# Kernel optimization log

Measured on AMD Instinct MI355X. Metric: run time of the kernel, lower is better.

Reference implementation:

```python
import jax, jax.numpy as jnp
import numpy as np

BETA = 1.0
B, S, D = 4, 4096, 1024


def setup_inputs() -> dict:
    key = jax.random.key(0)
    k_x, k_q, k_k, k_v = jax.random.split(key, 4)
    scale = 1.0 / np.sqrt(D)  # nn.Linear-like init scale
    x = jax.random.normal(k_x, (B, S, D), dtype=jnp.float32)
    Wq = jax.random.uniform(k_q, (D, D), dtype=jnp.float32, minval=-scale, maxval=scale)
    Wk = jax.random.uniform(k_k, (D, D), dtype=jnp.float32, minval=-scale, maxval=scale)
    Wv = jax.random.uniform(k_v, (D, D), dtype=jnp.float32, minval=-scale, maxval=scale)
    return {"x": x, "Wq": Wq, "Wk": Wk, "Wv": Wv}


def reference(x, Wq, Wk, Wv):
    # nn.Linear(bias=False): y = x @ W.T
    q = jnp.einsum('bsd,ed->bse', x, Wq)
    k = jnp.einsum('bsd,ed->bse', x, Wk)
    v = jnp.einsum('bsd,ed->bse', x, Wv)
    scores = jnp.einsum('bqd,bkd->bqk', q, k)          # [B, S, S]
    attn = jax.nn.softmax(BETA * scores, axis=-1)
    attended = jnp.einsum('bqk,bkd->bqd', attn, v)
    y = attended + x
    return y / jnp.linalg.norm(y, axis=-1, keepdims=True)
```

## Files before the change

### kernel.cpp

```cpp
#include <hip/hip_runtime.h>

typedef unsigned short u16;
typedef _Float16 half8 __attribute__((ext_vector_type(8)));
typedef __attribute__((ext_vector_type(4))) float f32x4;

constexpr int NB = 4;
constexpr int S  = 4096;
constexpr int D  = 1024;

__device__ __forceinline__ u16 h2u(_Float16 h) {
    union { _Float16 h; u16 u; } v; v.h = h; return v.u;
}

__device__ __forceinline__ void async16(const void* g, void* l) {
    __builtin_amdgcn_global_load_lds(
        (const __attribute__((address_space(1))) unsigned int*)g,
        (__attribute__((address_space(3))) unsigned int*)l, 16, 0, 0);
}

#define BAR()  __builtin_amdgcn_s_barrier()
#define SFEN() __builtin_amdgcn_sched_barrier(0)

#define MF(AF, BF, QM, QN)                                                     \
  do {                                                                         \
    _Pragma("unroll") for (int m_ = 0; m_ < 4; ++m_)                           \
    _Pragma("unroll") for (int n_ = 0; n_ < 2; ++n_)                           \
    _Pragma("unroll") for (int k_ = 0; k_ < 2; ++k_)                           \
      acc[(QM)*4 + m_][(QN)*2 + n_] = __builtin_amdgcn_mfma_f32_16x16x32_f16(  \
          AF[m_][k_], BF[n_][k_], acc[(QM)*4 + m_][(QN)*2 + n_], 0, 0, 0);     \
  } while (0)

#define GHALF(RA, RB, OA, OB, KO, KN)                                          \
  {                                               \
    _Pragma("unroll") for (int m_ = 0; m_ < 4; ++m_) {                         \
      a0[m_][0] = rdA(RA, 0, m_, 0); a0[m_][1] = rdA(RA, 0, m_, 1); }          \
    _Pragma("unroll") for (int n_ = 0; n_ < 2; ++n_) {                         \
      b0[n_][0] = rdB(RB, 0, n_, 0); b0[n_][1] = rdB(RB, 0, n_, 1); }          \
    issue(Am, OA, rsA + 64, KO);                                               \
    BAR();                                                                     \
    __builtin_amdgcn_s_setprio(1); MF(a0, b0, 0, 0);                           \
    __builtin_amdgcn_s_setprio(0);                                             \
    asm volatile("s_waitcnt vmcnt(6)" ::: "memory");                           \
    BAR(); SFEN();                                                             \
                                                  \
    _Pragma("unroll") for (int n_ = 0; n_ < 2; ++n_) {                         \
      b1[n_][0] = rdB(RB, 1, n_, 0); b1[n_][1] = rdB(RB, 1, n_, 1); }          \
    issue(Bm, OB, rsB + 32, KO);                                               \
    BAR();                                                                     \
    __builtin_amdgcn_s_setprio(1); MF(a0, b1, 0, 1);                           \
    __builtin_amdgcn_s_setprio(0);                                             \
    BAR(); SFEN();                                                             \
                                                  \
    _Pragma("unroll") for (int m_ = 0; m_ < 4; ++m_) {                         \
      a1[m_][0] = rdA(RA, 1, m_, 0); a1[m_][1] = rdA(RA, 1, m_, 1); }          \
    issue(Am, RA, rsA, KN);                                                    \
    BAR();                                                                     \
    __builtin_amdgcn_s_setprio(1); MF(a1, b0, 1, 0);                           \
    __builtin_amdgcn_s_setprio(0);                                             \
    BAR(); SFEN();                                                             \
                                                  \
    issue(Bm, RB, rsB, KN);                                                    \
    BAR();                                                                     \
    __builtin_amdgcn_s_setprio(1); MF(a1, b1, 1, 1);                           \
    __builtin_amdgcn_s_setprio(0);                                             \
    asm volatile("s_waitcnt vmcnt(8)" ::: "memory");                           \
    BAR(); SFEN();                                                             \
  }

__device__ __forceinline__ void gemm256(
    const u16* __restrict__ Am, const u16* __restrict__ Bm, const int K,
    u16* lds, f32x4 acc[8][4])
{
    const int tid  = threadIdx.x;
    const int lane = tid & 63;
    const int w    = tid >> 6;
    const int wm   = w >> 2;
    const int wn   = w & 3;
    const int quad = lane >> 4;
    const int lrow = lane & 15;
    const int s7   = lrow & 7;
    const int rl   = lane >> 3;
    const int gc8  = ((lane & 7) ^ rl) * 8;
    const int rsA  = ((w >> 2) << 7) + ((w & 3) << 4);
    const int rsB  = ((w >> 1) << 6) + ((w & 1) << 4);

    u16* const As0 = lds;
    u16* const Bs0 = lds + 16384;
    u16* const As1 = lds + 32768;
    u16* const Bs1 = lds + 49152;

    auto issue = [&](const u16* M, u16* dst, int rs, int k0) {
        async16(M + (size_t)(rs + rl) * K + k0 + gc8,
                dst + (size_t)(rs)     * 64 + (size_t)lane * 8);
        async16(M + (size_t)(rs + 8 + rl) * K + k0 + gc8,
                dst + (size_t)(rs + 8) * 64 + (size_t)lane * 8);
    };
    auto rdA = [&](const u16* buf, int qm, int m, int kk) -> half8 {
        return *(const half8*)(buf + (wm * 128 + qm * 64 + m * 16 + lrow) * 64
                                   + (((kk << 2) + quad) ^ s7) * 8);
    };
    auto rdB = [&](const u16* buf, int qn, int n, int kk) -> half8 {
        return *(const half8*)(buf + (wn * 64 + qn * 32 + n * 16 + lrow) * 64
                                   + (((kk << 2) + quad) ^ s7) * 8);
    };

    issue(Am, As0, rsA,      0);
    issue(Bm, Bs0, rsB,      0);
    issue(Am, As0, rsA + 64, 0);
    issue(Bm, Bs0, rsB + 32, 0);
    issue(Am, As1, rsA,      64);
    issue(Bm, Bs1, rsB,      64);
    asm volatile("s_waitcnt vmcnt(8)" ::: "memory");
    BAR(); SFEN();

    half8 a0[4][2], a1[4][2], b0[2][2], b1[2][2];
    const int kmask = K - 1;
    const int NI = K >> 7;
    for (int it = 0; it < NI; ++it) {
        const int kb  = it << 7;
        const int t1k = (kb + 64)  & kmask;
        const int t2k = (kb + 128) & kmask;
        const int t3k = (kb + 192) & kmask;
        GHALF(As0, Bs0, As1, Bs1, t1k, t2k)
        GHALF(As1, Bs1, As0, Bs0, t2k, t3k)
    }
}

__global__ __launch_bounds__(256) void cvt_kernel(
    const float* __restrict__ in, u16* __restrict__ out, int n8)
{
    const int i = blockIdx.x * 256 + threadIdx.x;
    if (i >= n8) return;
    const float4 a = *(const float4*)(in + (size_t)i * 8);
    const float4 b = *(const float4*)(in + (size_t)i * 8 + 4);
    half8 h;
    h[0] = (_Float16)a.x; h[1] = (_Float16)a.y;
    h[2] = (_Float16)a.z; h[3] = (_Float16)a.w;
    h[4] = (_Float16)b.x; h[5] = (_Float16)b.y;
    h[6] = (_Float16)b.z; h[7] = (_Float16)b.w;
    *(half8*)(out + (size_t)i * 8) = h;
}

__global__ __launch_bounds__(512, 2) void qkv_kernel(
    const u16* __restrict__ x16, const u16* __restrict__ W16,
    u16* __restrict__ Q, u16* __restrict__ Kb, u16* __restrict__ V)
{
    __shared__ __align__(16) u16 lds[65536];
    const int tile_m = blockIdx.x * 256;
    const int tile_n = blockIdx.y * 256;
    const u16* W = W16 + (size_t)blockIdx.z * D * D;
    u16* out = (blockIdx.z == 0) ? Q : (blockIdx.z == 1) ? Kb : V;

    f32x4 acc[8][4];
#pragma unroll
    for (int i = 0; i < 8; ++i)
#pragma unroll
        for (int j = 0; j < 4; ++j) acc[i][j] = (f32x4)0.0f;

    gemm256(x16 + (size_t)tile_m * D, W + (size_t)tile_n * D, D, lds, acc);

    const int tid = threadIdx.x, lane = tid & 63, w = tid >> 6;
    const int quad = lane >> 4, lrow = lane & 15;
    const int wm = w >> 2, wn = w & 3;
#pragma unroll
    for (int mi = 0; mi < 8; ++mi)
#pragma unroll
        for (int r = 0; r < 4; ++r) {
            const int row = tile_m + wm * 128 + mi * 16 + quad * 4 + r;
#pragma unroll
            for (int ni = 0; ni < 4; ++ni) {
                const int col = tile_n + wn * 64 + ni * 16 + lrow;
                out[(size_t)row * D + col] = h2u((_Float16)acc[mi][ni][r]);
            }
        }
}

__global__ __launch_bounds__(256) void transpose_v(
    const u16* __restrict__ V, u16* __restrict__ Vt)
{
    __shared__ u16 t[64][72];
    const int sg = blockIdx.x * 64;
    const int b  = sg >> 12;
    const int s0 = sg & (S - 1);
    const int e0 = blockIdx.y * 64;
    const int tid = threadIdx.x;
#pragma unroll
    for (int p = 0; p < 2; ++p) {
        const int v  = tid + 256 * p;
        const int sr = v >> 3, sc = (v & 7) * 8;
        half8 vec = *(const half8*)(V + (size_t)(sg + sr) * D + e0 + sc);
        *(half8*)&t[sr][sc] = vec;
    }
    __syncthreads();
#pragma unroll
    for (int p = 0; p < 2; ++p) {
        const int v  = tid + 256 * p;
        const int e  = v >> 3, s8 = (v & 7) * 8;
        u16 o[8];
#pragma unroll
        for (int j = 0; j < 8; ++j) o[j] = t[s8 + j][e];
        *(uint4*)(Vt + (size_t)b * D * S + (size_t)(e0 + e) * S + s0 + s8) = *(const uint4*)o;
    }
}

__global__ __launch_bounds__(512, 2) void scores_kernel(
    const u16* __restrict__ Q, const u16* __restrict__ Kb, u16* __restrict__ P)
{
    __shared__ __align__(16) u16 lds[65536];
    const int b = blockIdx.z;
    const int tile_m = blockIdx.x * 256;
    const int tile_n = blockIdx.y * 256;
    const u16* Ab = Q  + (size_t)b * S * D + (size_t)tile_m * D;
    const u16* Bv = Kb + (size_t)b * S * D + (size_t)tile_n * D;

    f32x4 acc[8][4];
#pragma unroll
    for (int i = 0; i < 8; ++i)
#pragma unroll
        for (int j = 0; j < 4; ++j) acc[i][j] = (f32x4)0.0f;

    gemm256(Ab, Bv, D, lds, acc);

    u16* Pb = P + (size_t)b * S * S;
    const int tid = threadIdx.x, lane = tid & 63, w = tid >> 6;
    const int quad = lane >> 4, lrow = lane & 15;
    const int wm = w >> 2, wn = w & 3;
#pragma unroll
    for (int mi = 0; mi < 8; ++mi)
#pragma unroll
        for (int r = 0; r < 4; ++r) {
            const int row = tile_m + wm * 128 + mi * 16 + quad * 4 + r;
#pragma unroll
            for (int ni = 0; ni < 4; ++ni) {
                const int col = tile_n + wn * 64 + ni * 16 + lrow;
                Pb[(size_t)row * S + col] = h2u((_Float16)acc[mi][ni][r]);
            }
        }
}

__global__ __launch_bounds__(256) void softmax_kernel(u16* __restrict__ P)
{
    const size_t row = blockIdx.x;
    u16* p = P + row * S;
    const int tid = threadIdx.x;

    half8 h0 = *(const half8*)(p + tid * 16);
    half8 h1 = *(const half8*)(p + tid * 16 + 8);
    float v[16];
#pragma unroll
    for (int i = 0; i < 8; ++i) { v[i] = (float)h0[i]; v[8 + i] = (float)h1[i]; }

    float m = v[0];
#pragma unroll
    for (int i = 1; i < 16; ++i) m = fmaxf(m, v[i]);
#pragma unroll
    for (int off = 32; off > 0; off >>= 1) m = fmaxf(m, __shfl_xor(m, off));

    __shared__ float redm[4], reds[4];
    const int wid = tid >> 6;
    if ((tid & 63) == 0) redm[wid] = m;
    __syncthreads();
    m = fmaxf(fmaxf(redm[0], redm[1]), fmaxf(redm[2], redm[3]));

    float e[16], s = 0.f;
#pragma unroll
    for (int i = 0; i < 16; ++i) { e[i] = __expf(v[i] - m); s += e[i]; }
#pragma unroll
    for (int off = 32; off > 0; off >>= 1) s += __shfl_xor(s, off);
    if ((tid & 63) == 0) reds[wid] = s;
    __syncthreads();
    s = reds[0] + reds[1] + reds[2] + reds[3];
    const float inv = 1.0f / s;

#pragma unroll
    for (int i = 0; i < 8; ++i) {
        h0[i] = (_Float16)(e[i] * inv);
        h1[i] = (_Float16)(e[8 + i] * inv);
    }
    *(half8*)(p + tid * 16)     = h0;
    *(half8*)(p + tid * 16 + 8) = h1;
}

__global__ __launch_bounds__(512, 2) void pv_kernel(
    const u16* __restrict__ P, const u16* __restrict__ Vt,
    const float* __restrict__ x, float* __restrict__ y)
{
    __shared__ __align__(16) u16 lds[65536];
    const int b = blockIdx.z;
    const int tile_m = blockIdx.x * 256;
    const int tile_n = blockIdx.y * 256;
    const u16* Ab = P  + (size_t)b * S * S + (size_t)tile_m * S;
    const u16* Bv = Vt + (size_t)b * D * S + (size_t)tile_n * S;

    f32x4 acc[8][4];
#pragma unroll
    for (int i = 0; i < 8; ++i)
#pragma unroll
        for (int j = 0; j < 4; ++j) acc[i][j] = (f32x4)0.0f;

    gemm256(Ab, Bv, S, lds, acc);

    const int tid = threadIdx.x, lane = tid & 63, w = tid >> 6;
    const int quad = lane >> 4, lrow = lane & 15;
    const int wm = w >> 2, wn = w & 3;

#pragma unroll
    for (int mi = 0; mi < 8; ++mi)
#pragma unroll
        for (int r = 0; r < 4; ++r) {
            const int row = tile_m + wm * 128 + mi * 16 + quad * 4 + r;
            const size_t base = ((size_t)b * S + row) * D;
#pragma unroll
            for (int ni = 0; ni < 4; ++ni) {
                const int col = tile_n + wn * 64 + ni * 16 + lrow;
                y[base + col] = acc[mi][ni][r] + x[base + col];
            }
        }
}

__global__ __launch_bounds__(256) void normalize_kernel(float* __restrict__ y)
{
    const size_t row = blockIdx.x;
    const int tid = threadIdx.x;
    float4* p = (float4*)(y + row * D) + tid;

    float4 v = *p;
    float ss = v.x * v.x + v.y * v.y + v.z * v.z + v.w * v.w;
#pragma unroll
    for (int off = 32; off > 0; off >>= 1) ss += __shfl_xor(ss, off);

    __shared__ float red[4];
    const int wid = tid >> 6;
    if ((tid & 63) == 0) red[wid] = ss;
    __syncthreads();
    const float inv = rsqrtf(red[0] + red[1] + red[2] + red[3]);

    v.x *= inv; v.y *= inv; v.z *= inv; v.w *= inv;
    *p = v;
}

extern "C" void kernel_launch(void* const* d_in, const int* in_sizes, int n_in,
                              void* d_out, int out_size, void* d_ws, size_t ws_size,
                              hipStream_t stream) {
    const float* x  = (const float*)d_in[0];
    const float* Wq = (const float*)d_in[1];
    const float* Wk = (const float*)d_in[2];
    const float* Wv = (const float*)d_in[3];
    float* out = (float*)d_out;

    char* ws = (char*)d_ws;
    const size_t MB = 1ull << 20;
    u16* Q   = (u16*)(ws);
    u16* Kb  = (u16*)(ws + 32 * MB);
    u16* Vt  = (u16*)(ws + 64 * MB);
    u16* P   = (u16*)(ws + 96 * MB);
    u16* V   = P;
    u16* x16 = Vt;
    u16* W16 = (u16*)(ws + 218 * MB);

    dim3 blk(256);
    dim3 blk2(512);
    cvt_kernel <<<dim3(NB * S * D / 8 / 256), blk, 0, stream>>>(x,  x16, NB * S * D / 8);
    cvt_kernel <<<dim3(D * D / 8 / 256), blk, 0, stream>>>(Wq, W16,             D * D / 8);
    cvt_kernel <<<dim3(D * D / 8 / 256), blk, 0, stream>>>(Wk, W16 + (size_t)D * D, D * D / 8);
    cvt_kernel <<<dim3(D * D / 8 / 256), blk, 0, stream>>>(Wv, W16 + (size_t)2 * D * D, D * D / 8);

    qkv_kernel    <<<dim3(NB * S / 256, D / 256, 3), blk2, 0, stream>>>(x16, W16, Q, Kb, V);
    transpose_v   <<<dim3(NB * S / 64, D / 64), blk, 0, stream>>>(V, Vt);
    scores_kernel <<<dim3(S / 256, S / 256, NB), blk2, 0, stream>>>(Q, Kb, P);
    softmax_kernel<<<dim3(NB * S), blk, 0, stream>>>(P);
    pv_kernel     <<<dim3(S / 256, D / 256, NB), blk2, 0, stream>>>(P, Vt, x, out);
    normalize_kernel<<<dim3(NB * S), blk, 0, stream>>>(out);
}
```

Measured before the change: 537.8 us.

## Restructure GEMM main loop barriers, precompute LDS pointers, and swizzle block order for XCDs

The GEMM inner loop now issues LDS fragment reads for the next sub-step before each barrier instead of after, removes one barrier per quarter-step, and waits with a tighter vmcnt. LDS read addresses are precomputed as per-thread base pointers with constant offsets, replacing the per-read index arithmetic. All three GEMM kernels remap the linear block id so consecutive blocks on the same XCD handle neighbouring tiles, aiming for better L2 reuse. Fewer barriers raise the risk of LDS read/write races if the async-load waits are not sufficient.

Result: slower. 549.7 us (+2.2%).

```diff
diff --git a/kernel.cpp b/kernel.cpp
--- a/kernel.cpp
+++ b/kernel.cpp
@@ -30,40 +30,40 @@
           AF[m_][k_], BF[n_][k_], acc[(QM)*4 + m_][(QN)*2 + n_], 0, 0, 0);     \
   } while (0)
 
-#define GHALF(RA, RB, OA, OB, KO, KN)                                          \
-  {                                               \
-    _Pragma("unroll") for (int m_ = 0; m_ < 4; ++m_) {                         \
-      a0[m_][0] = rdA(RA, 0, m_, 0); a0[m_][1] = rdA(RA, 0, m_, 1); }          \
-    _Pragma("unroll") for (int n_ = 0; n_ < 2; ++n_) {                         \
-      b0[n_][0] = rdB(RB, 0, n_, 0); b0[n_][1] = rdB(RB, 0, n_, 1); }          \
-    issue(Am, OA, rsA + 64, KO);                                               \
-    BAR();                                                                     \
+#define RDA(dst, bp0, bp1, qm)                                                 \
+  _Pragma("unroll") for (int m_ = 0; m_ < 4; ++m_) {                           \
+    dst[m_][0] = *(const half8*)(bp0 + (qm) * 4096 + m_ * 1024);               \
+    dst[m_][1] = *(const half8*)(bp1 + (qm) * 4096 + m_ * 1024); }
+#define RDB(dst, bp0, bp1, qn)                                                 \
+  _Pragma("unroll") for (int n_ = 0; n_ < 2; ++n_) {                           \
+    dst[n_][0] = *(const half8*)(bp0 + (qn) * 2048 + n_ * 1024);               \
+    dst[n_][1] = *(const half8*)(bp1 + (qn) * 2048 + n_ * 1024); }
+
+#define HALF(RAd, RBd, OAd, OBd, rA0, rA1, rB0, rB1, KO, KN)                   \
+  {                                              \
+    RDA(a0, rA0, rA1, 0)                                                       \
+    RDB(b0, rB0, rB1, 0)                                                       \
+    issue(Am, OAd, rsA + 64, KO);                                              \
     __builtin_amdgcn_s_setprio(1); MF(a0, b0, 0, 0);                           \
     __builtin_amdgcn_s_setprio(0);                                             \
-    asm volatile("s_waitcnt vmcnt(6)" ::: "memory");                           \
+    RDB(b1, rB0, rB1, 1)                                                       \
     BAR(); SFEN();                                                             \
-                                                  \
-    _Pragma("unroll") for (int n_ = 0; n_ < 2; ++n_) {                         \
-      b1[n_][0] = rdB(RB, 1, n_, 0); b1[n_][1] = rdB(RB, 1, n_, 1); }          \
-    issue(Bm, OB, rsB + 32, KO);                                               \
-    BAR();                                                                     \
+                                                      \
+    issue(Bm, OBd, rsB + 32, KO);                                              \
     __builtin_amdgcn_s_setprio(1); MF(a0, b1, 0, 1);                           \
     __builtin_amdgcn_s_setprio(0);                                             \
+    RDA(a1, rA0, rA1, 1)                                                       \
     BAR(); SFEN();                                                             \
-                                                  \
-    _Pragma("unroll") for (int m_ = 0; m_ < 4; ++m_) {                         \
-      a1[m_][0] = rdA(RA, 1, m_, 0); a1[m_][1] = rdA(RA, 1, m_, 1); }          \
-    issue(Am, RA, rsA, KN);                                                    \
-    BAR();                                                                     \
+                                                      \
+    issue(Am, RAd, rsA, KN);                                                   \
     __builtin_amdgcn_s_setprio(1); MF(a1, b0, 1, 0);                           \
     __builtin_amdgcn_s_setprio(0);                                             \
     BAR(); SFEN();                                                             \
-                                                  \
-    issue(Bm, RB, rsB, KN);                                                    \
-    BAR();                                                                     \
+                                                      \
+    issue(Bm, RBd, rsB, KN);                                                   \
     __builtin_amdgcn_s_setprio(1); MF(a1, b1, 1, 1);                           \
     __builtin_amdgcn_s_setprio(0);                                             \
-    asm volatile("s_waitcnt vmcnt(8)" ::: "memory");                           \
+    asm volatile("s_waitcnt vmcnt(4)" ::: "memory");                           \
     BAR(); SFEN();                                                             \
   }
 
@@ -81,13 +81,24 @@
     const int s7   = lrow & 7;
     const int rl   = lane >> 3;
     const int gc8  = ((lane & 7) ^ rl) * 8;
-    const int rsA  = ((w >> 2) << 7) + ((w & 3) << 4);
+    const int rsA  = (wm << 7) + ((w & 3) << 4);
     const int rsB  = ((w >> 1) << 6) + ((w & 1) << 4);
 
     u16* const As0 = lds;
     u16* const Bs0 = lds + 16384;
     u16* const As1 = lds + 32768;
     u16* const Bs1 = lds + 49152;
+
+    const int lt0 = lrow * 64 + ((quad ^ s7) * 8);
+    const int lt1 = lrow * 64 + (((4 + quad) ^ s7) * 8);
+    const u16* const bA00 = As0 + wm * 8192 + lt0;
+    const u16* const bA01 = As0 + wm * 8192 + lt1;
+    const u16* const bA10 = As1 + wm * 8192 + lt0;
+    const u16* const bA11 = As1 + wm * 8192 + lt1;
+    const u16* const bB00 = Bs0 + wn * 4096 + lt0;
+    const u16* const bB01 = Bs0 + wn * 4096 + lt1;
+    const u16* const bB10 = Bs1 + wn * 4096 + lt0;
+    const u16* const bB11 = Bs1 + wn * 4096 + lt1;
 
     auto issue = [&](const u16* M, u16* dst, int rs, int k0) {
         async16(M + (size_t)(rs + rl) * K + k0 + gc8,
@@ -95,14 +106,6 @@
         async16(M + (size_t)(rs + 8 + rl) * K + k0 + gc8,
                 dst + (size_t)(rs + 8) * 64 + (size_t)lane * 8);
     };
-    auto rdA = [&](const u16* buf, int qm, int m, int kk) -> half8 {
-        return *(const half8*)(buf + (wm * 128 + qm * 64 + m * 16 + lrow) * 64
-                                   + (((kk << 2) + quad) ^ s7) * 8);
-    };
-    auto rdB = [&](const u16* buf, int qn, int n, int kk) -> half8 {
-        return *(const half8*)(buf + (wn * 64 + qn * 32 + n * 16 + lrow) * 64
-                                   + (((kk << 2) + quad) ^ s7) * 8);
-    };
 
     issue(Am, As0, rsA,      0);
     issue(Bm, Bs0, rsB,      0);
@@ -110,19 +113,19 @@
     issue(Bm, Bs0, rsB + 32, 0);
     issue(Am, As1, rsA,      64);
     issue(Bm, Bs1, rsB,      64);
-    asm volatile("s_waitcnt vmcnt(8)" ::: "memory");
+    asm volatile("s_waitcnt vmcnt(4)" ::: "memory");
     BAR(); SFEN();
 
     half8 a0[4][2], a1[4][2], b0[2][2], b1[2][2];
-    const int kmask = K - 1;
+    const int km = K - 1;
     const int NI = K >> 7;
     for (int it = 0; it < NI; ++it) {
         const int kb  = it << 7;
-        const int t1k = (kb + 64)  & kmask;
-        const int t2k = (kb + 128) & kmask;
-        const int t3k = (kb + 192) & kmask;
-        GHALF(As0, Bs0, As1, Bs1, t1k, t2k)
-        GHALF(As1, Bs1, As0, Bs0, t2k, t3k)
+        const int t1k = (kb + 64)  & km;
+        const int t2k = (kb + 128) & km;
+        const int t3k = (kb + 192) & km;
+        HALF(As0, Bs0, As1, Bs1, bA00, bA01, bB00, bB01, t1k, t2k)
+        HALF(As1, Bs1, As0, Bs0, bA10, bA11, bB10, bB11, t2k, t3k)
     }
 }
 
@@ -146,10 +149,14 @@
     u16* __restrict__ Q, u16* __restrict__ Kb, u16* __restrict__ V)
 {
     __shared__ __align__(16) u16 lds[65536];
-    const int tile_m = blockIdx.x * 256;
-    const int tile_n = blockIdx.y * 256;
-    const u16* W = W16 + (size_t)blockIdx.z * D * D;
-    u16* out = (blockIdx.z == 0) ? Q : (blockIdx.z == 1) ? Kb : V;
+    const int lin = blockIdx.x + (blockIdx.y << 6) + (blockIdx.z << 8);
+    const int swz = (lin & 7) * 96 + (lin >> 3);
+    const int bx = swz & 63, by = (swz >> 6) & 3, bz = swz >> 8;
+
+    const int tile_m = bx * 256;
+    const int tile_n = by * 256;
+    const u16* W = W16 + (size_t)bz * D * D;
+    u16* out = (bz == 0) ? Q : (bz == 1) ? Kb : V;
 
     f32x4 acc[8][4];
 #pragma unroll
@@ -207,9 +214,13 @@
     const u16* __restrict__ Q, const u16* __restrict__ Kb, u16* __restrict__ P)
 {
     __shared__ __align__(16) u16 lds[65536];
-    const int b = blockIdx.z;
-    const int tile_m = blockIdx.x * 256;
-    const int tile_n = blockIdx.y * 256;
+    const int lin = blockIdx.x + ((blockIdx.y + (blockIdx.z << 4)) << 4);
+    const int swz = ((lin & 7) << 7) + (lin >> 3);
+    const int bx = swz & 15, by = (swz >> 4) & 15, bz = swz >> 8;
+
+    const int b = bz;
+    const int tile_m = bx * 256;
+    const int tile_n = by * 256;
     const u16* Ab = Q  + (size_t)b * S * D + (size_t)tile_m * D;
     const u16* Bv = Kb + (size_t)b * S * D + (size_t)tile_n * D;
 
@@ -286,9 +297,13 @@
     const float* __restrict__ x, float* __restrict__ y)
 {
     __shared__ __align__(16) u16 lds[65536];
-    const int b = blockIdx.z;
-    const int tile_m = blockIdx.x * 256;
-    const int tile_n = blockIdx.y * 256;
+    const int lin = blockIdx.x + (blockIdx.y << 4) + (blockIdx.z << 6);
+    const int swz = ((lin & 7) << 5) + (lin >> 3);
+    const int bx = swz & 15, by = (swz >> 4) & 3, bz = swz >> 6;
+
+    const int b = bz;
+    const int tile_m = bx * 256;
+    const int tile_n = by * 256;
     const u16* Ab = P  + (size_t)b * S * S + (size_t)tile_m * S;
     const u16* Bv = Vt + (size_t)b * D * S + (size_t)tile_n * S;
 
```
